# Performance work log

Hardware: AMD Instinct MI355X
Metric: run time of the kernel (lower is better)

## Reference

```python
import jax, jax.numpy as jnp
import numpy as np

H, KV, D, EPS = 32, 8, 128, 1e-6
G = H // KV  # kv groups = 4
ROPE_THETA = 5000000.0


def _rms_norm(x, gamma):
    # x: (..., D)
    return x * jax.lax.rsqrt(jnp.mean(x * x, axis=-1, keepdims=True) + EPS) * gamma


def _rotate_half(x):
    x1, x2 = jnp.split(x, 2, axis=-1)
    return jnp.concatenate([-x2, x1], axis=-1)


def _apply_rope(x, cos, sin):
    # x: (b, h, s, D); cos/sin: (b, s, 1, D) -> (b, 1, s, D)
    cos = jnp.transpose(cos, (0, 2, 1, 3))
    sin = jnp.transpose(sin, (0, 2, 1, 3))
    return x * cos + _rotate_half(x) * sin


def setup_inputs() -> dict:
    key = jax.random.key(0)
    ks = jax.random.split(key, 8)
    b, s, hid = 2, 2048, 2560
    hidden = jax.random.normal(ks[0], (b, s, hid), dtype=jnp.float32)
    # realistic RoPE tables (half-split convention matching _rotate_half)
    inv_freq = 1.0 / (ROPE_THETA ** (np.arange(0, D, 2, dtype=np.float32) / D))  # (D/2,)
    pos = np.arange(s, dtype=np.float32)
    freqs = np.outer(pos, inv_freq)                     # (s, D/2)
    emb = np.concatenate([freqs, freqs], axis=-1)       # (s, D)
    cos = jnp.broadcast_to(jnp.asarray(np.cos(emb))[None, :, None, :], (b, s, 1, D))
    sin = jnp.broadcast_to(jnp.asarray(np.sin(emb))[None, :, None, :], (b, s, 1, D))
    sc = 1.0 / np.sqrt(hid)
    wq = jax.random.normal(ks[1], (H * D, hid), dtype=jnp.float32) * sc
    wk = jax.random.normal(ks[2], (KV * D, hid), dtype=jnp.float32) * sc
    wv = jax.random.normal(ks[3], (KV * D, hid), dtype=jnp.float32) * sc
    wo = jax.random.normal(ks[4], (hid, H * D), dtype=jnp.float32) * (1.0 / np.sqrt(H * D))
    q_gamma = jnp.ones((D,), dtype=jnp.float32)
    k_gamma = jnp.ones((D,), dtype=jnp.float32)
    return {"hidden": hidden, "cos": cos, "sin": sin, "wq": wq, "wk": wk,
            "wv": wv, "wo": wo, "q_gamma": q_gamma, "k_gamma": k_gamma}


def reference(hidden, cos, sin, wq, wk, wv, wo, q_gamma, k_gamma):
    b, s, _ = hidden.shape
    # projections -> (b, heads, s, D)
    q = (hidden @ wq.T).reshape(b, s, H, D).transpose(0, 2, 1, 3)
    k = (hidden @ wk.T).reshape(b, s, KV, D).transpose(0, 2, 1, 3)
    v = (hidden @ wv.T).reshape(b, s, KV, D).transpose(0, 2, 1, 3)
    # QK-RMSNorm over head_dim
    q = _rms_norm(q, q_gamma)
    k = _rms_norm(k, k_gamma)
    # RoPE
    q = _apply_rope(q, cos, sin)
    k = _apply_rope(k, cos, sin)
    new_k, new_v = k, v  # kv cache (no prior cache)
    # GQA attention without materializing expanded K/V
    qg = q.reshape(b, KV, G, s, D)
    scale = 1.0 / np.sqrt(D)
    scores = jnp.einsum('bkgqd,bkld->bkgql', qg, k) * scale  # (b,KV,G,s,s)
    causal = jnp.tril(jnp.ones((s, s), dtype=bool))
    scores = jnp.where(causal, scores, jnp.finfo(scores.dtype).min)
    probs = jax.nn.softmax(scores, axis=-1)
    out = jnp.einsum('bkgql,bkld->bkgqd', probs, v)          # (b,KV,G,s,D)
    out = out.reshape(b, H, s, D).transpose(0, 2, 1, 3).reshape(b, s, H * D)
    return (out @ wo.T, new_k, new_v)
```

## Files before the change

### kernel.cpp

```cpp
#include <hip/hip_runtime.h>
#include <stdint.h>

typedef unsigned short u16;
typedef __attribute__((ext_vector_type(8))) short short8;
typedef __attribute__((ext_vector_type(4))) float f32x4;

#define MFMA_BF16(a,b,c) __builtin_amdgcn_mfma_f32_16x16x32_bf16((a),(b),(c),0,0,0)

#define S_BARRIER()  asm volatile("s_barrier" ::: "memory")
#define WAIT_LGKM0() asm volatile("s_waitcnt lgkmcnt(0)" ::: "memory")
#define WAIT_VM(N)   asm volatile("s_waitcnt vmcnt(" #N ")" ::: "memory")

__device__ __forceinline__ u16 f2bf(float x) {
    uint32_t u = __builtin_bit_cast(uint32_t, x);
    u += 0x7fffu + ((u >> 16) & 1u);
    return (u16)(u >> 16);
}
__device__ __forceinline__ float bf2f(u16 u) {
    return __builtin_bit_cast(float, (uint32_t)u << 16);
}
__device__ __forceinline__ void glds16(const void* g, void* lds) {
    __builtin_amdgcn_global_load_lds((const __attribute__((address_space(1))) void*)g,
                                     (__attribute__((address_space(3))) void*)lds,
                                     16, 0, 0);
}

__device__ __forceinline__ void cvt4(const float* __restrict__ s,
                                     u16* __restrict__ d, int i) {
    float4 v = *(const float4*)(s + i);
    ushort4 o;
    o.x = f2bf(v.x); o.y = f2bf(v.y); o.z = f2bf(v.z); o.w = f2bf(v.w);
    *(ushort4*)(d + i) = o;
}
__global__ __launch_bounds__(256) void cvt_all(
        const float* __restrict__ s0, u16* __restrict__ d0,
        const float* __restrict__ s1, u16* __restrict__ d1,
        const float* __restrict__ s2, u16* __restrict__ d2,
        const float* __restrict__ s3, u16* __restrict__ d3,
        const float* __restrict__ s4, u16* __restrict__ d4)
{
    int i = (blockIdx.x * 256 + threadIdx.x) * 4;
    if      (i < 10485760) cvt4(s0, d0, i);
    else if (i < 20971520) cvt4(s1, d1, i - 10485760);
    else if (i < 23592960) cvt4(s2, d2, i - 20971520);
    else if (i < 26214400) cvt4(s3, d3, i - 23592960);
    else if (i < 36700160) cvt4(s4, d4, i - 26214400);
}

template<int MH, int NH>
__device__ __forceinline__ void mm16(f32x4 (&acc)[8][4],
                                     const short8 (&a)[4][2],
                                     const short8 (&b)[2][2]) {
#pragma unroll
    for (int k2 = 0; k2 < 2; k2++)
#pragma unroll
        for (int mi = 0; mi < 4; mi++)
#pragma unroll
            for (int nj = 0; nj < 2; nj++)
                acc[MH * 4 + mi][NH * 2 + nj] =
                    MFMA_BF16(a[mi][k2], b[nj][k2], acc[MH * 4 + mi][NH * 2 + nj]);
}

template<bool BF16_OUT>
__global__ __launch_bounds__(512, 2) void gemm8(const u16* __restrict__ A,
                                                const u16* __restrict__ B,
                                                void* __restrict__ Cv,
                                                int K, int lda, int ldb, int ldc,
                                                int ntn)
{
    __shared__ __align__(16) u16 Sm[65536];
    const int t = threadIdx.x;
    const int w = t >> 6, l = t & 63;
    const int lrow = l & 15, lk = l >> 4;
    const int wm = w >> 2, wn = w & 3;

    const int nwg = (int)gridDim.x;
    const int cpx = nwg >> 3;
    const int id = (int)blockIdx.x;
    const int sw = (id & 7) * cpx + (id >> 3);
    const int tm = sw / ntn, tn = sw - tm * ntn;
    const int m0 = tm * 256, n0 = tn * 256;

    const int nkt = K >> 6;
    const size_t laneOffA = (size_t)(w * 16 + (l >> 3)) * lda + (((l & 7) ^ (l >> 3)) * 8);
    const size_t laneOffB = (size_t)(w * 16 + (l >> 3)) * ldb + (((l & 7) ^ (l >> 3)) * 8);
    const u16* Ag = A + (size_t)m0 * lda;
    const u16* Bg = B + (size_t)n0 * ldb;

    auto STAGE_A = [&](int kt, int slot, int h) {
#pragma unroll
        for (int j = 0; j < 2; j++)
            glds16(Ag + laneOffA + (size_t)(h * 128 + j * 8) * lda + kt * 64,
                   (char*)Sm + slot * 65536 + h * 16384 + w * 2048 + j * 1024);
    };
    auto STAGE_B = [&](int kt, int slot, int h) {
#pragma unroll
        for (int j = 0; j < 2; j++)
            glds16(Bg + laneOffB + (size_t)(h * 128 + j * 8) * ldb + kt * 64,
                   (char*)Sm + 32768 + slot * 65536 + h * 16384 + w * 2048 + j * 1024);
    };
    auto READ_A = [&](short8 (&a)[4][2], int slot, int rb) {
#pragma unroll
        for (int mi = 0; mi < 4; mi++)
#pragma unroll
            for (int k2 = 0; k2 < 2; k2++) {
                int row = rb + mi * 16 + lrow;
                a[mi][k2] = *(const short8*)&Sm[slot * 32768 + row * 64 +
                                                (((k2 * 4 + lk) ^ (lrow & 7)) * 8)];
            }
    };
    auto READ_B = [&](short8 (&b)[2][2], int slot, int rb) {
#pragma unroll
        for (int nj = 0; nj < 2; nj++)
#pragma unroll
            for (int k2 = 0; k2 < 2; k2++) {
                int row = rb + nj * 16 + lrow;
                b[nj][k2] = *(const short8*)&Sm[slot * 32768 + 16384 + row * 64 +
                                                (((k2 * 4 + lk) ^ (lrow & 7)) * 8)];
            }
    };

    f32x4 acc[8][4];
#pragma unroll
    for (int i = 0; i < 8; i++)
#pragma unroll
        for (int j = 0; j < 4; j++) acc[i][j] = (f32x4){0.f, 0.f, 0.f, 0.f};
    short8 aF0[4][2], aF1[4][2], bF0[2][2], bF1[2][2];

    STAGE_A(0, 0, 0); STAGE_A(0, 0, 1);
    STAGE_B(0, 0, 0); STAGE_B(0, 0, 1);
    const int k1 = (nkt > 1) ? 1 : 0;
    STAGE_A(k1, 1, 0); STAGE_A(k1, 1, 1);
    WAIT_VM(4);
    S_BARRIER();

    for (int kt = 0; kt < nkt; ++kt) {
        const int slot = kt & 1, nslot = slot ^ 1;
        const int ktB = (kt + 1 < nkt) ? kt + 1 : kt;
        const int ktA = (kt + 2 < nkt) ? kt + 2 : kt;
        READ_A(aF0, slot, wm * 128);
        READ_B(bF0, slot, wn * 64);
        STAGE_B(ktB, nslot, 0);
        S_BARRIER();
        WAIT_LGKM0();
        __builtin_amdgcn_sched_barrier(0);
        __builtin_amdgcn_s_setprio(1);
        mm16<0, 0>(acc, aF0, bF0);
        __builtin_amdgcn_s_setprio(0);
        S_BARRIER();
        READ_A(aF1, slot, wm * 128 + 64);
        STAGE_B(ktB, nslot, 1);
        S_BARRIER();
        WAIT_LGKM0();
        __builtin_amdgcn_sched_barrier(0);
        __builtin_amdgcn_s_setprio(1);
        mm16<1, 0>(acc, aF1, bF0);
        __builtin_amdgcn_s_setprio(0);
        S_BARRIER();
        READ_B(bF1, slot, wn * 64 + 32);
        STAGE_A(ktA, slot, 0);
        S_BARRIER();
        WAIT_LGKM0();
        __builtin_amdgcn_sched_barrier(0);
        __builtin_amdgcn_s_setprio(1);
        mm16<1, 1>(acc, aF1, bF1);
        __builtin_amdgcn_s_setprio(0);
        S_BARRIER();
        STAGE_A(ktA, slot, 1);
        S_BARRIER();
        __builtin_amdgcn_s_setprio(1);
        mm16<0, 1>(acc, aF0, bF1);
        __builtin_amdgcn_s_setprio(0);
        WAIT_VM(4);
        S_BARRIER();
    }
    WAIT_VM(0);

#pragma unroll
    for (int mi = 0; mi < 8; mi++) {
#pragma unroll
        for (int r = 0; r < 4; r++) {
            int row = m0 + wm * 128 + mi * 16 + lk * 4 + r;
#pragma unroll
            for (int nj = 0; nj < 4; nj++) {
                int col = n0 + wn * 64 + nj * 16 + lrow;
                float v = acc[mi][nj][r];
                if (BF16_OUT) ((u16*)Cv)[(size_t)row * ldc + col] = f2bf(v);
                else          ((float*)Cv)[(size_t)row * ldc + col] = v;
            }
        }
    }
}

__global__ __launch_bounds__(512, 2) void gemm192(const u16* __restrict__ A,
                                                  const u16* __restrict__ B,
                                                  u16* __restrict__ C,
                                                  int K, int lda, int ldb, int ldc)
{
    __shared__ __align__(16) u16 Sm[57344];
    const int t = threadIdx.x;
    const int w = t >> 6, l = t & 63;
    const int lrow = l & 15, lk = l >> 4;
    const int wm = w >> 2, wn = w & 3;

    const int nwg = (int)gridDim.x;
    const int cpx = nwg >> 3;
    const int id = (int)blockIdx.x;
    const int sw = (id & 7) * cpx + (id >> 3);
    const int tm = sw >> 5, tn = sw & 31;
    const int m0 = tm * 256, n0 = tn * 192;

    const int nkt = K >> 6;
    const size_t laneOffA = (size_t)(w * 16 + (l >> 3)) * lda + (((l & 7) ^ (l >> 3)) * 8);
    const size_t laneOffB = (size_t)(w * 24 + (l >> 3)) * ldb + (((l & 7) ^ (l >> 3)) * 8);
    const u16* Ag = A + (size_t)m0 * lda;
    const u16* Bg = B + (size_t)n0 * ldb;

    auto STAGE_A = [&](int kt, int slot, int h) {
#pragma unroll
        for (int j = 0; j < 2; j++)
            glds16(Ag + laneOffA + (size_t)(h * 128 + j * 8) * lda + kt * 64,
                   (char*)Sm + slot * 32768 + h * 16384 + w * 2048 + j * 1024);
    };
    auto STAGE_B1 = [&](int kt, int slot, int b) {
        glds16(Bg + laneOffB + (size_t)(b * 8) * ldb + kt * 64,
               (char*)Sm + 65536 + slot * 24576 + w * 3072 + b * 1024);
    };
    auto READ_A = [&](short8 (&a)[4][2], int slot, int rb) {
#pragma unroll
        for (int mi = 0; mi < 4; mi++)
#pragma unroll
            for (int k2 = 0; k2 < 2; k2++) {
                int row = rb + mi * 16 + lrow;
                a[mi][k2] = *(const short8*)&Sm[slot * 16384 + row * 64 +
                                                (((k2 * 4 + lk) ^ (lrow & 7)) * 8)];
            }
    };
    auto READ_B2 = [&](short8 (&b)[2][2], int slot) {
#pragma unroll
        for (int nj = 0; nj < 2; nj++)
#pragma unroll
            for (int k2 = 0; k2 < 2; k2++) {
                int row = wn * 48 + nj * 16 + lrow;
                b[nj][k2] = *(const short8*)&Sm[32768 + slot * 12288 + row * 64 +
                                                (((k2 * 4 + lk) ^ (lrow & 7)) * 8)];
            }
    };
    auto READ_B1 = [&](short8 (&b)[1][2], int slot) {
#pragma unroll
        for (int k2 = 0; k2 < 2; k2++) {
            int row = wn * 48 + 32 + lrow;
            b[0][k2] = *(const short8*)&Sm[32768 + slot * 12288 + row * 64 +
                                           (((k2 * 4 + lk) ^ (lrow & 7)) * 8)];
        }
    };

    f32x4 acc[8][3];
#pragma unroll
    for (int i = 0; i < 8; i++)
#pragma unroll
        for (int j = 0; j < 3; j++) acc[i][j] = (f32x4){0.f, 0.f, 0.f, 0.f};
    short8 aF0[4][2], aF1[4][2], bF0[2][2], bF1[1][2];

    STAGE_A(0, 0, 0); STAGE_A(0, 0, 1);
    STAGE_B1(0, 0, 0); STAGE_B1(0, 0, 1); STAGE_B1(0, 0, 2);
    const int k1 = (nkt > 1) ? 1 : 0;
    STAGE_A(k1, 1, 0); STAGE_A(k1, 1, 1);
    WAIT_VM(4);
    S_BARRIER();

    for (int kt = 0; kt < nkt; ++kt) {
        const int slot = kt & 1, nslot = slot ^ 1;
        const int ktB = (kt + 1 < nkt) ? kt + 1 : kt;
        const int ktA = (kt + 2 < nkt) ? kt + 2 : kt;
        READ_A(aF0, slot, wm * 128);
        READ_B2(bF0, slot);
        STAGE_B1(ktB, nslot, 0);
        S_BARRIER();
        WAIT_LGKM0();
        __builtin_amdgcn_sched_barrier(0);
        __builtin_amdgcn_s_setprio(1);
#pragma unroll
        for (int k2 = 0; k2 < 2; k2++)
#pragma unroll
            for (int mi = 0; mi < 4; mi++)
#pragma unroll
                for (int nj = 0; nj < 2; nj++)
                    acc[mi][nj] = MFMA_BF16(aF0[mi][k2], bF0[nj][k2], acc[mi][nj]);
        __builtin_amdgcn_s_setprio(0);
        S_BARRIER();
        READ_A(aF1, slot, wm * 128 + 64);
        STAGE_B1(ktB, nslot, 1); STAGE_B1(ktB, nslot, 2);
        S_BARRIER();
        WAIT_LGKM0();
        __builtin_amdgcn_sched_barrier(0);
        __builtin_amdgcn_s_setprio(1);
#pragma unroll
        for (int k2 = 0; k2 < 2; k2++)
#pragma unroll
            for (int mi = 0; mi < 4; mi++)
#pragma unroll
                for (int nj = 0; nj < 2; nj++)
                    acc[4 + mi][nj] = MFMA_BF16(aF1[mi][k2], bF0[nj][k2], acc[4 + mi][nj]);
        __builtin_amdgcn_s_setprio(0);
        S_BARRIER();
        READ_B1(bF1, slot);
        STAGE_A(ktA, slot, 0);
        S_BARRIER();
        WAIT_LGKM0();
        __builtin_amdgcn_sched_barrier(0);
        __builtin_amdgcn_s_setprio(1);
#pragma unroll
        for (int k2 = 0; k2 < 2; k2++)
#pragma unroll
            for (int mi = 0; mi < 4; mi++)
                acc[4 + mi][2] = MFMA_BF16(aF1[mi][k2], bF1[0][k2], acc[4 + mi][2]);
        __builtin_amdgcn_s_setprio(0);
        S_BARRIER();
        STAGE_A(ktA, slot, 1);
        S_BARRIER();
        __builtin_amdgcn_s_setprio(1);
#pragma unroll
        for (int k2 = 0; k2 < 2; k2++)
#pragma unroll
            for (int mi = 0; mi < 4; mi++)
                acc[mi][2] = MFMA_BF16(aF0[mi][k2], bF1[0][k2], acc[mi][2]);
        __builtin_amdgcn_s_setprio(0);
        WAIT_VM(4);
        S_BARRIER();
    }
    WAIT_VM(0);

#pragma unroll
    for (int mi = 0; mi < 8; mi++) {
#pragma unroll
        for (int r = 0; r < 4; r++) {
            int row = m0 + wm * 128 + mi * 16 + lk * 4 + r;
#pragma unroll
            for (int nj = 0; nj < 3; nj++) {
                int col = n0 + wn * 48 + nj * 16 + lrow;
                C[(size_t)row * ldc + col] = f2bf(acc[mi][nj][r]);
            }
        }
    }
}

__global__ __launch_bounds__(256) void norm_rope_qk(const u16* __restrict__ qkv,
        const float* __restrict__ cosb, const float* __restrict__ sinb,
        const float* __restrict__ qg, const float* __restrict__ kg,
        u16* __restrict__ qb, u16* __restrict__ kb, float* __restrict__ k_out)
{
    const int idx = blockIdx.x * 4 + (threadIdx.x >> 6);
    const int l = threadIdx.x & 63;
    const int tok = idx / 40, hd = idx - tok * 40;
    const int b = tok >> 11, pos = tok & 2047;
    const u16* row = qkv + (size_t)tok * 6144 + hd * 128;
    ushort2 xr = *(const ushort2*)(row + 2 * l);
    float xa = bf2f(xr.x), xb = bf2f(xr.y);
    float ss = xa * xa + xb * xb;
#pragma unroll
    for (int m = 1; m < 64; m <<= 1) ss += __shfl_xor(ss, m, 64);
    float rn = rsqrtf(ss * (1.0f / 128.0f) + 1e-6f);

    const float* gm = (hd < 32) ? qg : kg;
    float2 g = *(const float2*)(gm + 2 * l);
    float na = xa * rn * g.x, nb = xb * rn * g.y;
    float pa = __shfl_xor(na, 32, 64);
    float pb = __shfl_xor(nb, 32, 64);
    float2 c = *(const float2*)(cosb + (size_t)tok * 128 + 2 * l);
    float2 s = *(const float2*)(sinb + (size_t)tok * 128 + 2 * l);
    float sgn = (l < 32) ? -1.0f : 1.0f;
    float ya = na * c.x + sgn * pa * s.x;
    float yb = nb * c.y + sgn * pb * s.y;
    if (hd < 32) {
        const float qs = 0.08838834764831845f;
        size_t base = (((size_t)b * 32 + hd) * 2048 + pos) * 128;
        ushort2 o; o.x = f2bf(ya * qs); o.y = f2bf(yb * qs);
        *(ushort2*)(qb + base + 2 * l) = o;
    } else {
        int kv = hd - 32;
        size_t base = (((size_t)b * 8 + kv) * 2048 + pos) * 128;
        *(float2*)(k_out + base + 2 * l) = make_float2(ya, yb);
        ushort2 o; o.x = f2bf(ya); o.y = f2bf(yb);
        *(ushort2*)(kb + base + 2 * l) = o;
    }
}

__global__ __launch_bounds__(256) void v_pack(const u16* __restrict__ qkv,
        float* __restrict__ v_out, u16* __restrict__ vtb)
{
    __shared__ __align__(16) u16 T[64 * 128];
    const int pb = blockIdx.x, bkv = blockIdx.y;
    const int b = bkv >> 3, kv = bkv & 7;
    const int p0 = pb * 64;
    const int t = threadIdx.x;
    const int pos = t >> 2, ch4 = t & 3;
    const u16* src = qkv + (size_t)(b * 2048 + p0 + pos) * 6144 + (40 + kv) * 128 + ch4 * 32;
    float* vdst = v_out + ((size_t)bkv * 2048 + p0 + pos) * 128 + ch4 * 32;
#pragma unroll
    for (int j = 0; j < 4; j++) {
        short8 x = *(const short8*)(src + j * 8);
        float4 f0, f1;
        f0.x = bf2f(x[0]); f0.y = bf2f(x[1]); f0.z = bf2f(x[2]); f0.w = bf2f(x[3]);
        f1.x = bf2f(x[4]); f1.y = bf2f(x[5]); f1.z = bf2f(x[6]); f1.w = bf2f(x[7]);
        *(float4*)(vdst + j * 8)     = f0;
        *(float4*)(vdst + j * 8 + 4) = f1;
        int slot = (ch4 * 4 + j) ^ (pos & 7);
        *(short8*)&T[pos * 128 + slot * 8] = x;
    }
    __syncthreads();
    const int d = t & 127, ph = t >> 7;
    u16* obase = vtb + ((size_t)bkv * 128 + d) * 2048 + p0 + ph * 32;
#pragma unroll
    for (int g = 0; g < 4; g++) {
        short8 tv;
#pragma unroll
        for (int jj = 0; jj < 8; jj++) {
            int pp = ph * 32 + g * 8 + jj;
            int slot = (d >> 3) ^ (pp & 7);
            tv[jj] = (short)T[pp * 128 + slot * 8 + (d & 7)];
        }
        *(short8*)(obase + g * 8) = tv;
    }
}

__global__ __launch_bounds__(256, 3) void attn_kernel(const u16* __restrict__ qb,
        const u16* __restrict__ kb, const u16* __restrict__ vtb,
        u16* __restrict__ ao)
{
    __shared__ __align__(16) u16 Ks[64 * 128];
    __shared__ __align__(16) u16 Vs[128 * 64];
    __shared__ __align__(16) u16 Ps[4][32 * 72];

    const int p = (int)blockIdx.x;
    const int g = (p & 7) + ((p >> 5) << 3);
    const int bh = g * 4 + ((p >> 3) & 3);
    const int b = bh >> 5, h = bh & 31;
    const int kvh = h >> 2;
    const int qt = (int)gridDim.y - 1 - (int)blockIdx.y;
    const int q0 = qt * 128;
    const int t = threadIdx.x, w = t >> 6, l = t & 63;
    const int lrow = l & 15, lk = l >> 4;

    const u16* qbase  = qb  + ((size_t)b * 32 + h)  * 2048 * 128;
    const u16* kbase  = kb  + ((size_t)b * 8 + kvh) * 2048 * 128;
    const u16* vtbase = vtb + ((size_t)b * 8 + kvh) * 128 * 2048;

    short8 qf[2][4];
#pragma unroll
    for (int m = 0; m < 2; m++) {
        const u16* qrow = qbase + (size_t)(q0 + w * 32 + m * 16 + lrow) * 128 + lk * 8;
#pragma unroll
        for (int ks = 0; ks < 4; ks++) qf[m][ks] = *(const short8*)(qrow + ks * 32);
    }

    f32x4 o[2][8];
#pragma unroll
    for (int m = 0; m < 2; m++)
#pragma unroll
        for (int i = 0; i < 8; i++) o[m][i] = (f32x4){0.f, 0.f, 0.f, 0.f};
    float lsum[2][4] = {{0.f,0.f,0.f,0.f},{0.f,0.f,0.f,0.f}};

    int kR[4], kG[4], vR[4], vG[4];
#pragma unroll
    for (int i = 0; i < 4; i++) {
        int c = i * 256 + t;
        kR[i] = c >> 4; kG[i] = (c & 15) ^ (kR[i] & 7);
        vR[i] = c >> 3; vG[i] = (c & 7)  ^ (vR[i] & 7);
    }
    char* Ksb = (char*)Ks + w * 1024;
    char* Vsb = (char*)Vs + w * 1024;
    u16* pw = &Ps[w][0];
    const int wrow_max = q0 + w * 32 + 31;

    const int nkt = 2 * qt + 2;
    for (int kt = 0; kt < nkt; kt++) {
        const int kv0 = kt * 64;
        __syncthreads();
#pragma unroll
        for (int i = 0; i < 4; i++)
            glds16(kbase + (size_t)(kv0 + kR[i]) * 128 + kG[i] * 8, Ksb + i * 4096);
#pragma unroll
        for (int i = 0; i < 4; i++)
            glds16(vtbase + (size_t)vR[i] * 2048 + kv0 + vG[i] * 8, Vsb + i * 4096);
        __syncthreads();

        if (kv0 > wrow_max) continue;

        f32x4 s[2][4];
#pragma unroll
        for (int m = 0; m < 2; m++)
#pragma unroll
            for (int i = 0; i < 4; i++) s[m][i] = (f32x4){0.f, 0.f, 0.f, 0.f};
        __builtin_amdgcn_s_setprio(1);
#pragma unroll
        for (int ks = 0; ks < 4; ks++) {
#pragma unroll
            for (int nt = 0; nt < 4; nt++) {
                int r = nt * 16 + lrow;
                int sl = (ks * 4 + lk) ^ (r & 7);
                short8 kf = *(const short8*)&Ks[r * 128 + sl * 8];
                s[0][nt] = MFMA_BF16(qf[0][ks], kf, s[0][nt]);
                s[1][nt] = MFMA_BF16(qf[1][ks], kf, s[1][nt]);
            }
        }
        __builtin_amdgcn_s_setprio(0);

#pragma unroll
        for (int m = 0; m < 2; m++) {
            const int rowbase = q0 + w * 32 + m * 16;
            if (kv0 + 63 > rowbase) {
#pragma unroll
                for (int nt = 0; nt < 4; nt++) {
                    int cg = kv0 + nt * 16 + lrow;
#pragma unroll
                    for (int r = 0; r < 4; r++)
                        if (cg > rowbase + lk * 4 + r) s[m][nt][r] = -1e30f;
                }
            }
#pragma unroll
            for (int nt = 0; nt < 4; nt++)
#pragma unroll
                for (int r = 0; r < 4; r++) {
                    float pv = __expf(s[m][nt][r]);
                    s[m][nt][r] = pv;
                    lsum[m][r] += pv;
                    pw[(m * 16 + lk * 4 + r) * 72 + nt * 16 + lrow] = f2bf(pv);
                }
        }
        asm volatile("s_waitcnt lgkmcnt(0)" ::: "memory");

        __builtin_amdgcn_s_setprio(1);
#pragma unroll
        for (int k2 = 0; k2 < 2; k2++) {
            short8 pf0 = *(const short8*)&pw[lrow * 72 + k2 * 32 + lk * 8];
            short8 pf1 = *(const short8*)&pw[(16 + lrow) * 72 + k2 * 32 + lk * 8];
#pragma unroll
            for (int nt = 0; nt < 8; nt++) {
                int rr = nt * 16 + lrow;
                int sl = (k2 * 4 + lk) ^ (rr & 7);
                short8 vf = *(const short8*)&Vs[rr * 64 + sl * 8];
                o[0][nt] = MFMA_BF16(pf0, vf, o[0][nt]);
                o[1][nt] = MFMA_BF16(pf1, vf, o[1][nt]);
            }
        }
        __builtin_amdgcn_s_setprio(0);
    }

#pragma unroll
    for (int m = 0; m < 2; m++)
#pragma unroll
        for (int r = 0; r < 4; r++) {
            float v = lsum[m][r];
            v += __shfl_xor(v, 1, 64);
            v += __shfl_xor(v, 2, 64);
            v += __shfl_xor(v, 4, 64);
            v += __shfl_xor(v, 8, 64);
            lsum[m][r] = 1.0f / v;
        }
#pragma unroll
    for (int m = 0; m < 2; m++)
#pragma unroll
        for (int nt = 0; nt < 8; nt++)
#pragma unroll
            for (int r = 0; r < 4; r++) {
                int tok = q0 + w * 32 + m * 16 + lk * 4 + r;
                size_t off = ((size_t)b * 2048 + tok) * 4096 + h * 128 + nt * 16 + lrow;
                ao[off] = f2bf(o[m][nt][r] * lsum[m][r]);
            }
}

extern "C" void kernel_launch(void* const* d_in, const int* in_sizes, int n_in,
                              void* d_out, int out_size, void* d_ws, size_t ws_size,
                              hipStream_t stream)
{
    (void)in_sizes; (void)n_in; (void)out_size; (void)ws_size;
    const float* hidden = (const float*)d_in[0];
    const float* cosb   = (const float*)d_in[1];
    const float* sinb   = (const float*)d_in[2];
    const float* wq     = (const float*)d_in[3];
    const float* wk     = (const float*)d_in[4];
    const float* wv     = (const float*)d_in[5];
    const float* wo     = (const float*)d_in[6];
    const float* qg     = (const float*)d_in[7];
    const float* kg     = (const float*)d_in[8];

    float* out   = (float*)d_out;
    float* k_out = out + (size_t)2 * 2048 * 2560;
    float* v_out = k_out + (size_t)2 * 8 * 2048 * 128;

    u16* hid_b = (u16*)d_ws;
    u16* w_b   = hid_b + 10485760;
    u16* wo_b  = w_b   + 15728640;
    u16* q_b   = wo_b  + 10485760;
    u16* k_b   = q_b   + 16777216;
    u16* vt_b  = k_b   + 4194304;
    u16* qkv_b = vt_b  + 4194304;
    u16* ao_b  = hid_b;

    cvt_all<<<35840, 256, 0, stream>>>(hidden, hid_b, wq, w_b,
                                       wk, w_b + 10485760, wv, w_b + 13107200,
                                       wo, wo_b);

    gemm192<<<dim3(512), 512, 0, stream>>>(hid_b, w_b, qkv_b,
                                           2560, 2560, 2560, 6144);
    norm_rope_qk<<<40960, 256, 0, stream>>>(qkv_b, cosb, sinb, qg, kg,
                                            q_b, k_b, k_out);
    v_pack<<<dim3(32, 16), 256, 0, stream>>>(qkv_b, v_out, vt_b);
    attn_kernel<<<dim3(64, 16), 256, 0, stream>>>(q_b, k_b, vt_b, ao_b);
    gemm8<false><<<dim3(160), 512, 0, stream>>>(ao_b, wo_b, out,
                                                4096, 4096, 4096, 2560, 10);
}
```

Measured before the change: 598.1 us.

## Split-K the output projection GEMM across two halves with a reduction pass

The final output projection GEMM is split along K into two halves, launching 320 workgroups instead of 160. The first half writes directly to the output and the second half writes to a scratch partial buffer that reuses the QKV workspace. A small elementwise kernel then adds the partial into the output. The aim is to fill more compute units on the 256-CU device, at the cost of an extra fp32 write/read pass over the output and one more launch.

```diff
diff --git a/kernel.cpp b/kernel.cpp
--- a/kernel.cpp
+++ b/kernel.cpp
@@ -61,12 +61,12 @@
                     MFMA_BF16(a[mi][k2], b[nj][k2], acc[MH * 4 + mi][NH * 2 + nj]);
 }
 
-template<bool BF16_OUT>
-__global__ __launch_bounds__(512, 2) void gemm8(const u16* __restrict__ A,
-                                                const u16* __restrict__ B,
-                                                void* __restrict__ Cv,
-                                                int K, int lda, int ldb, int ldc,
-                                                int ntn)
+__global__ __launch_bounds__(512, 2) void gemm8sk(const u16* __restrict__ A,
+                                                  const u16* __restrict__ B,
+                                                  float* __restrict__ outp,
+                                                  float* __restrict__ part,
+                                                  int Khalf, int lda, int ldb, int ldc,
+                                                  int ntn, int nhalf)
 {
     __shared__ __align__(16) u16 Sm[65536];
     const int t = threadIdx.x;
@@ -74,18 +74,23 @@
     const int lrow = l & 15, lk = l >> 4;
     const int wm = w >> 2, wn = w & 3;
 
-    const int nwg = (int)gridDim.x;
-    const int cpx = nwg >> 3;
-    const int id = (int)blockIdx.x;
+    const int idr = (int)blockIdx.x;
+    const int half = (idr >= nhalf) ? 1 : 0;
+    const int id = idr - half * nhalf;
+    const int cpx = nhalf >> 3;
     const int sw = (id & 7) * cpx + (id >> 3);
     const int tm = sw / ntn, tn = sw - tm * ntn;
     const int m0 = tm * 256, n0 = tn * 256;
 
-    const int nkt = K >> 6;
+    const u16* Ah = A + (size_t)half * Khalf;
+    const u16* Bh = B + (size_t)half * Khalf;
+    float* Cp = half ? part : outp;
+
+    const int nkt = Khalf >> 6;
     const size_t laneOffA = (size_t)(w * 16 + (l >> 3)) * lda + (((l & 7) ^ (l >> 3)) * 8);
     const size_t laneOffB = (size_t)(w * 16 + (l >> 3)) * ldb + (((l & 7) ^ (l >> 3)) * 8);
-    const u16* Ag = A + (size_t)m0 * lda;
-    const u16* Bg = B + (size_t)n0 * ldb;
+    const u16* Ag = Ah + (size_t)m0 * lda;
+    const u16* Bg = Bh + (size_t)n0 * ldb;
 
     auto STAGE_A = [&](int kt, int slot, int h) {
 #pragma unroll
@@ -184,12 +189,20 @@
 #pragma unroll
             for (int nj = 0; nj < 4; nj++) {
                 int col = n0 + wn * 64 + nj * 16 + lrow;
-                float v = acc[mi][nj][r];
-                if (BF16_OUT) ((u16*)Cv)[(size_t)row * ldc + col] = f2bf(v);
-                else          ((float*)Cv)[(size_t)row * ldc + col] = v;
-            }
-        }
-    }
+                Cp[(size_t)row * ldc + col] = acc[mi][nj][r];
+            }
+        }
+    }
+}
+
+__global__ __launch_bounds__(256) void addk(float* __restrict__ o,
+                                            const float* __restrict__ p)
+{
+    int i = (blockIdx.x * 256 + threadIdx.x) * 4;
+    float4 a = *(const float4*)(o + i);
+    float4 b = *(const float4*)(p + i);
+    a.x += b.x; a.y += b.y; a.z += b.z; a.w += b.w;
+    *(float4*)(o + i) = a;
 }
 
 __global__ __launch_bounds__(512, 2) void gemm192(const u16* __restrict__ A,
@@ -597,6 +610,7 @@
     u16* vt_b  = k_b   + 4194304;
     u16* qkv_b = vt_b  + 4194304;
     u16* ao_b  = hid_b;
+    float* part = (float*)qkv_b;
 
     cvt_all<<<35840, 256, 0, stream>>>(hidden, hid_b, wq, w_b,
                                        wk, w_b + 10485760, wv, w_b + 13107200,
@@ -608,6 +622,7 @@
                                             q_b, k_b, k_out);
     v_pack<<<dim3(32, 16), 256, 0, stream>>>(qkv_b, v_out, vt_b);
     attn_kernel<<<dim3(64, 16), 256, 0, stream>>>(q_b, k_b, vt_b, ao_b);
-    gemm8<false><<<dim3(160), 512, 0, stream>>>(ao_b, wo_b, out,
-                                                4096, 4096, 4096, 2560, 10);
-}
+    gemm8sk<<<dim3(320), 512, 0, stream>>>(ao_b, wo_b, out, part,
+                                           2048, 4096, 4096, 2560, 10, 160);
+    addk<<<10240, 256, 0, stream>>>(out, part);
+}
```

Result: slower. 625.6 us (+4.6%).
